# Kernel optimization log

Measured on AMD Instinct MI355X. Metric: run time of the kernel, lower is better.

## Reference

```python
import jax, jax.numpy as jnp
import numpy as np

EPS = 1e-6
LAMB = 0.1
ITERS = 3


def setup_inputs() -> dict:
    key = jax.random.key(0)
    k = jax.random.split(key, 6)
    bi, bt, R, W, D = 128, 128, 36, 50, 1024
    return {
        "img_cls": jax.random.normal(k[0], (bi, D), jnp.float32),
        "imgs": jax.random.normal(k[1], (bi, R, D), jnp.float32),
        "cap_cls": jax.random.normal(k[2], (bt, D), jnp.float32),
        "caps": jax.random.normal(k[3], (bt, W, D), jnp.float32),
        "img_lens": jax.random.randint(k[4], (bi,), 1, R + 1, jnp.int32),
        "cap_lens": jax.random.randint(k[5], (bt,), 1, W + 1, jnp.int32),
    }


def _bregman(cost, mask, r, c):
    # P = exp(-cost/lamb) (masked entries have cost=+inf -> P=0), then
    # iterative row/col rescaling toward marginals r, c.
    P = jnp.where(mask, jnp.exp(-cost / LAMB), 0.0)
    P = P / (jnp.sum(P, axis=(-2, -1), keepdims=True) + EPS)
    for _ in range(ITERS):
        u = P.sum(axis=-1) + EPS          # [bi,bt,R]
        P = P * (r / u)[..., None]
        v = P.sum(axis=-2) + EPS          # [bi,bt,W]
        P = P * (c / v)[:, :, None, :]
    return P


def reference(img_cls, imgs, cap_cls, caps, img_lens, cap_lens):
    imgs = imgs + EPS
    caps = caps + EPS
    # prepend cls token
    imgs = jnp.concatenate([img_cls[:, None, :], imgs], axis=1)   # [bi,R+1,D]
    caps = jnp.concatenate([cap_cls[:, None, :], caps], axis=1)   # [bt,W+1,D]
    imgs = imgs / jnp.linalg.norm(imgs, axis=-1, keepdims=True)
    caps = caps / jnp.linalg.norm(caps, axis=-1, keepdims=True)
    # fine-grained cosine sims: [bi, bt, R+1, W+1]
    fg_sims = jnp.einsum("ird,twd->itrw", imgs, caps)
    il = img_lens + 1
    cl = cap_lens + 1
    R1, W1 = imgs.shape[1], caps.shape[1]
    rmask = jnp.arange(R1)[None, :] < il[:, None]   # [bi,R+1]
    wmask = jnp.arange(W1)[None, :] < cl[:, None]   # [bt,W+1]
    mask = rmask[:, None, :, None] & wmask[None, :, None, :]  # [bi,bt,R+1,W+1]
    # _ave_init: uniform marginals over valid rows/cols
    rvalid = mask.any(axis=-1).astype(fg_sims.dtype)  # [bi,bt,R+1]
    cvalid = mask.any(axis=-2).astype(fg_sims.dtype)  # [bi,bt,W+1]
    r = rvalid / rvalid.sum(axis=-1, keepdims=True)
    c = cvalid / cvalid.sum(axis=-1, keepdims=True)
    cost = 1.0 - fg_sims
    tp = _bregman(cost, mask, r, c)
    sims = jnp.sum(fg_sims * tp * mask.astype(fg_sims.dtype), axis=(-2, -1))
    return sims  # [bi, bt]
```

## Files before the change

kernel.cpp:

```cpp
#include <hip/hip_runtime.h>
#include <hip/hip_fp16.h>

#define EPSF 1e-6f

typedef _Float16 f16x8 __attribute__((ext_vector_type(8)));
typedef float f32x4 __attribute__((ext_vector_type(4)));

#define BK 32
#define SMEM_BYTES 75776
#define BUF_BYTES 10240

#define AS1 __attribute__((address_space(1)))
#define AS3 __attribute__((address_space(3)))

#define VM_WAIT(N) asm volatile("s_waitcnt vmcnt(" #N ")" ::: "memory")
#define LGKM0()    asm volatile("s_waitcnt lgkmcnt(0)" ::: "memory")

__device__ __forceinline__ float wave_sum_fast(float x) {
    asm volatile(
        "s_nop 1\n\t"
        "v_add_f32 %0, %0, %0 quad_perm:[1,0,3,2] row_mask:0xf bank_mask:0xf bound_ctrl:0\n\t"
        "s_nop 1\n\t"
        "v_add_f32 %0, %0, %0 quad_perm:[2,3,0,1] row_mask:0xf bank_mask:0xf bound_ctrl:0\n\t"
        "s_nop 1\n\t"
        "v_add_f32 %0, %0, %0 row_half_mirror row_mask:0xf bank_mask:0xf bound_ctrl:0\n\t"
        "s_nop 1\n\t"
        "v_add_f32 %0, %0, %0 row_mirror row_mask:0xf bank_mask:0xf bound_ctrl:0\n\t"
        "s_nop 1\n\t"
        "v_add_f32 %0, %0, %0 row_bcast:15 row_mask:0xf bank_mask:0xf bound_ctrl:0\n\t"
        "s_nop 1\n\t"
        "v_add_f32 %0, %0, %0 row_bcast:31 row_mask:0xf bank_mask:0xf bound_ctrl:0"
        : "+v"(x));
    return __int_as_float(__builtin_amdgcn_readlane(__float_as_int(x), 63));
}

__global__ __launch_bounds__(256) void norm_kernel(
        const float* __restrict__ img_cls, const float* __restrict__ imgs,
        const float* __restrict__ cap_cls, const float* __restrict__ caps,
        __half* __restrict__ Ah, __half* __restrict__ Bh) {
    __shared__ float red[4];
    const int row = blockIdx.x;
    const int tid = threadIdx.x;

    const float* src = nullptr;
    __half* dsth;
    float eps_add = EPSF;
    if (row < 64 * 80) {
        const int g = row / 80, r = row % 80;
        dsth = Ah + (size_t)row * 1024 + tid * 4;
        int i = -1, rr = 0;
        if (r < 37)      { i = 2 * g;     rr = r; }
        else if (r < 74) { i = 2 * g + 1; rr = r - 37; }
        if (i >= 0) {
            if (rr == 0) { src = img_cls + (size_t)i * 1024; eps_add = 0.0f; }
            else         { src = imgs + ((size_t)i * 36 + (rr - 1)) * 1024; }
        }
    } else {
        const int row2 = row - 64 * 80;
        const int t = row2 >> 6, r = row2 & 63;
        const int n = r >> 4, fr = r & 15;
        const int kt = tid >> 3, q4 = (tid >> 1) & 3, j = (tid & 1) * 4;
        dsth = Bh + ((size_t)(t * 32 + kt) * 4 + n) * 512 + (q4 * 16 + fr) * 8 + j;
        if (r == 0)       { src = cap_cls + (size_t)t * 1024; eps_add = 0.0f; }
        else if (r <= 50) { src = caps + ((size_t)t * 50 + (r - 1)) * 1024; }
    }

    if (src == nullptr) {
        ushort4 z; z.x = z.y = z.z = z.w = 0;
        *reinterpret_cast<ushort4*>(dsth) = z;
        return;
    }

    float4 v = reinterpret_cast<const float4*>(src)[tid];
    v.x += eps_add; v.y += eps_add; v.z += eps_add; v.w += eps_add;
    float ss = v.x * v.x + v.y * v.y + v.z * v.z + v.w * v.w;
    #pragma unroll
    for (int m = 1; m <= 32; m <<= 1) ss += __shfl_xor(ss, m);
    if ((tid & 63) == 0) red[tid >> 6] = ss;
    __syncthreads();
    const float tot = red[0] + red[1] + red[2] + red[3];
    const float rn = 1.0f / sqrtf(tot);

    ushort4 o;
    o.x = __half_as_ushort(__float2half(v.x * rn));
    o.y = __half_as_ushort(__float2half(v.y * rn));
    o.z = __half_as_ushort(__float2half(v.z * rn));
    o.w = __half_as_ushort(__float2half(v.w * rn));
    *reinterpret_cast<ushort4*>(dsth) = o;
}

__device__ __forceinline__ void stage_octA(const __half* __restrict__ Ag,
                                           __half* buf, int kb, int o, size_t lofs) {
    const __half* src = Ag + (size_t)o * 16384 + kb + lofs;
    __builtin_amdgcn_global_load_lds((const AS1 void*)src,
                                     (AS3 void*)(buf + o * 512), 16, 0, 0);
}

__device__ __forceinline__ void stage_A(const __half* __restrict__ Ag,
                                        __half* buf, int kb, int wave, size_t lofs) {
    stage_octA(Ag, buf, kb, wave, lofs);
    if (wave < 2) stage_octA(Ag, buf, kb, wave + 8, lofs);
}

__device__ __forceinline__ void ds_af(const __half* buf, int wm2, int fr, int q4,
                                      f16x8 af[5]) {
    const int soff = ((q4 ^ ((fr >> 1) & 3)) * 8);
    #pragma unroll
    for (int m = 0; m < 5; ++m) {
        const int R = wm2 * 80 + m * 16 + fr;
        af[m] = *reinterpret_cast<const f16x8*>(buf + R * BK + soff);
    }
}

__device__ __forceinline__ void load_bf(const __half* __restrict__ Bgw, int kt,
                                        f16x8 bf[2]) {
    const __half* p = Bgw + (size_t)kt * 2048;
    bf[0] = *reinterpret_cast<const f16x8*>(p);
    bf[1] = *reinterpret_cast<const f16x8*>(p + 512);
}

__device__ __forceinline__ void mfma_cluster(f32x4 acc[5][2], const f16x8 af[5],
                                             const f16x8 bf[2]) {
    __builtin_amdgcn_s_setprio(1);
    #pragma unroll
    for (int m = 0; m < 5; ++m)
        #pragma unroll
        for (int n = 0; n < 2; ++n)
            acc[m][n] = __builtin_amdgcn_mfma_f32_16x16x32_f16(af[m], bf[n], acc[m][n], 0, 0, 0);
    __builtin_amdgcn_s_setprio(0);
}

__global__ __launch_bounds__(512, 4) void fused_kernel(
        const __half* __restrict__ Ah, const __half* __restrict__ Bh,
        const int* __restrict__ img_lens, const int* __restrict__ cap_lens,
        float* __restrict__ out) {
    __shared__ __align__(16) char smem[SMEM_BYTES];
    __half* lds0 = reinterpret_cast<__half*>(smem);
    __half* lds1 = reinterpret_cast<__half*>(smem + BUF_BYTES);
    __half* lds2 = reinterpret_cast<__half*>(smem + 2 * BUF_BYTES);
    __half* lds3 = reinterpret_cast<__half*>(smem + 3 * BUF_BYTES);

    const int idx = blockIdx.x;
    const int xcd = idx & 7;
    const int within = idx >> 3;
    const int bx = within >> 3;
    const int by = xcd * 8 + (within & 7);

    const int tid = threadIdx.x;
    const int wave = tid >> 6;
    const int lane = tid & 63;
    const int wm2 = wave >> 2;
    const int wn2 = wave & 3;
    const int fr = lane & 15;
    const int q4 = lane >> 4;

    const __half* Ag = Ah + (size_t)bx * 160 * 1024;
    const __half* Bgw = Bh + (size_t)(2 * by + (wn2 >> 1)) * 65536
                           + (size_t)((wn2 & 1) * 2) * 512 + lane * 8;

    const int rsub = lane >> 2;
    const int segsrc = (lane & 3) ^ ((lane >> 3) & 3);
    const size_t lofs = (size_t)rsub * 1024 + (size_t)(segsrc * 8);

    f32x4 acc[5][2];
    #pragma unroll
    for (int m = 0; m < 5; ++m)
        #pragma unroll
        for (int n = 0; n < 2; ++n) {
            f32x4 z = {0.0f, 0.0f, 0.0f, 0.0f};
            acc[m][n] = z;
        }

    f16x8 bfA[2], bfB[2];

    stage_A(Ag, lds0, 0, wave, lofs);
    load_bf(Bgw, 0, bfA);
    stage_A(Ag, lds1, BK, wave, lofs);
    load_bf(Bgw, 1, bfB);
    stage_A(Ag, lds2, 2 * BK, wave, lofs);
    if (wave < 2) { VM_WAIT(6); } else { VM_WAIT(4); }
    __builtin_amdgcn_s_barrier();

    #define GEMM_TILE(KT, RDBUF, STBUF, CUR)                          \
    {                                                                 \
        f16x8 af[5];                                                  \
        ds_af((RDBUF), wm2, fr, q4, af);                              \
        mfma_cluster(acc, af, (CUR));                                 \
        load_bf(Bgw, (KT) + 2, (CUR));                                \
        LGKM0();                                                      \
        stage_A(Ag, (STBUF), ((KT) + 3) * BK, wave, lofs);            \
        if (wave < 2) { VM_WAIT(6); } else { VM_WAIT(4); }            \
        __builtin_amdgcn_s_barrier();                                 \
    }

    #pragma unroll 1
    for (int kt = 0; kt < 28; kt += 4) {
        GEMM_TILE(kt,     lds0, lds3, bfA);
        GEMM_TILE(kt + 1, lds1, lds0, bfB);
        GEMM_TILE(kt + 2, lds2, lds1, bfA);
        GEMM_TILE(kt + 3, lds3, lds2, bfB);
    }
    GEMM_TILE(28, lds0, lds3, bfA);
    #undef GEMM_TILE

    {
        f16x8 af[5];
        ds_af(lds1, wm2, fr, q4, af);
        mfma_cluster(acc, af, bfB);
        load_bf(Bgw, 31, bfB);
        LGKM0();
        if (wave < 2) { VM_WAIT(4); } else { VM_WAIT(3); }
        __builtin_amdgcn_s_barrier();
    }
    {
        f16x8 af[5];
        ds_af(lds2, wm2, fr, q4, af);
        mfma_cluster(acc, af, bfA);
        LGKM0();
        VM_WAIT(2);
        __builtin_amdgcn_s_barrier();
    }
    {
        f16x8 af[5];
        ds_af(lds3, wm2, fr, q4, af);
        VM_WAIT(0);
        mfma_cluster(acc, af, bfB);
    }

    __syncthreads();

    float* fgall = reinterpret_cast<float*>(smem);
    const int tt = wn2 >> 1;
    {
        #pragma unroll
        for (int m = 0; m < 5; ++m) {
            #pragma unroll
            for (int q = 0; q < 4; ++q) {
                const int Rl = m * 16 + q4 * 4 + q;
                const int s = (Rl >= 37) ? 1 : 0;
                const int sr = Rl - 37 * s;
                const bool valid = (Rl < 74);
                const int rg = (wm2 * 2 + s) * 2 + tt;
                const int sw = ((sr >> 2) & 3) << 4;
                #pragma unroll
                for (int n = 0; n < 2; ++n) {
                    const int sc = (wn2 & 1) * 32 + n * 16 + fr;
                    if (valid)
                        fgall[rg * 2368 + sr * 64 + (sc ^ sw)] = acc[m][n][q];
                }
            }
        }
    }
    __syncthreads();

    {
        float* fg = fgall + wave * 2368;
        const int i = 4 * bx + (wave >> 1);
        const int t = 2 * by + (wave & 1);
        const int il = img_lens[i] + 1;
        const int cl = cap_lens[t] + 1;
        const bool vcol = lane < cl;

        #define FGR(r_) fg[(r_) * 64 + (lane ^ ((((r_) >> 2) & 3) << 4))]
        #define CEND(c_) ((((c_) * 8 + 8) < 37) ? ((c_) * 8 + 8) : 37)

        float P[37];
        #pragma unroll
        for (int r = 0; r < 37; ++r) P[r] = 0.0f;

        float ts[4] = {0.f, 0.f, 0.f, 0.f};
        #pragma unroll
        for (int c = 0; c < 5; ++c) {
            if (c * 8 < il) {
                #pragma unroll
                for (int r = c * 8; r < CEND(c); ++r) {
                    const float f = FGR(r);
                    const bool act = (r < il) && vcol;
                    const float pe = act ? __expf((f - 1.0f) * 10.0f) : 0.0f;
                    P[r] = pe;
                    ts[r & 3] += pe;
                }
            }
        }
        float tot = (ts[0] + ts[1]) + (ts[2] + ts[3]);
        tot = wave_sum_fast(tot);
        const float s0 = __builtin_amdgcn_rcpf(tot + EPSF);
        #pragma unroll
        for (int c = 0; c < 5; ++c) {
            if (c * 8 < il) {
                #pragma unroll
                for (int r = c * 8; r < CEND(c); ++r) P[r] *= s0;
            }
        }

        const float rmarg = 1.0f / (float)il;
        const float cmarg = 1.0f / (float)cl;
        float csave = 0.0f;
        for (int it = 0; it < 3; ++it) {
            #pragma unroll
            for (int c = 0; c < 5; ++c) {
                if (c * 8 < il) {
                    #pragma unroll
                    for (int r = c * 8; r < CEND(c); ++r) {
                        const float u = wave_sum_fast(P[r]);
                        P[r] *= rmarg * __builtin_amdgcn_rcpf(u + EPSF);
                    }
                }
            }
            float vs[4] = {EPSF, 0.f, 0.f, 0.f};
            #pragma unroll
            for (int c = 0; c < 5; ++c) {
                if (c * 8 < il) {
                    #pragma unroll
                    for (int r = c * 8; r < CEND(c); ++r) vs[r & 3] += P[r];
                }
            }
            const float v = (vs[0] + vs[1]) + (vs[2] + vs[3]);
            const float cs = vcol ? cmarg * __builtin_amdgcn_rcpf(v) : 0.0f;
            if (it < 2) {
                #pragma unroll
                for (int c = 0; c < 5; ++c) {
                    if (c * 8 < il) {
                        #pragma unroll
                        for (int r = c * 8; r < CEND(c); ++r) P[r] *= cs;
                    }
                }
            } else {
                csave = cs;
            }
        }

        float ls[4] = {0.f, 0.f, 0.f, 0.f};
        #pragma unroll
        for (int c = 0; c < 5; ++c) {
            if (c * 8 < il) {
                #pragma unroll
                for (int r = c * 8; r < CEND(c); ++r) {
                    const float f = FGR(r);
                    const float fm = (r < il) ? f : 0.0f;
                    ls[r & 3] = fmaf(fm, P[r], ls[r & 3]);
                }
            }
        }
        float local = csave * ((ls[0] + ls[1]) + (ls[2] + ls[3]));
        local = wave_sum_fast(local);
        if (lane == 0) out[i * 128 + t] = local;
        #undef FGR
        #undef CEND
    }
}

extern "C" void kernel_launch(void* const* d_in, const int* in_sizes, int n_in,
                              void* d_out, int out_size, void* d_ws, size_t ws_size,
                              hipStream_t stream) {
    const float* img_cls  = (const float*)d_in[0];
    const float* imgs     = (const float*)d_in[1];
    const float* cap_cls  = (const float*)d_in[2];
    const float* caps     = (const float*)d_in[3];
    const int*   img_lens = (const int*)d_in[4];
    const int*   cap_lens = (const int*)d_in[5];
    float* out = (float*)d_out;

    __half* Ah = (__half*)d_ws;
    __half* Bh = Ah + (size_t)64 * 80 * 1024;

    norm_kernel<<<64 * 80 + 128 * 64, 256, 0, stream>>>(img_cls, imgs, cap_cls, caps, Ah, Bh);
    fused_kernel<<<2048, 512, 0, stream>>>(Ah, Bh, img_lens, cap_lens, out);
}
```

Baseline: 148.5 us.

## Double GEMM K-tile to 64 with triple-buffered LDS staging

```diff
diff --git a/kernel.cpp b/kernel.cpp
--- a/kernel.cpp
+++ b/kernel.cpp
@@ -6,9 +6,9 @@
 typedef _Float16 f16x8 __attribute__((ext_vector_type(8)));
 typedef float f32x4 __attribute__((ext_vector_type(4)));
 
-#define BK 32
+#define BK 64
 #define SMEM_BYTES 75776
-#define BUF_BYTES 10240
+#define BUF_BYTES 20480
 
 #define AS1 __attribute__((address_space(1)))
 #define AS3 __attribute__((address_space(3)))
@@ -91,7 +91,7 @@
 
 __device__ __forceinline__ void stage_octA(const __half* __restrict__ Ag,
                                            __half* buf, int kb, int o, size_t lofs) {
-    const __half* src = Ag + (size_t)o * 16384 + kb + lofs;
+    const __half* src = Ag + (size_t)o * 8192 + kb + lofs;
     __builtin_amdgcn_global_load_lds((const AS1 void*)src,
                                      (AS3 void*)(buf + o * 512), 16, 0, 0);
 }
@@ -99,12 +99,14 @@
 __device__ __forceinline__ void stage_A(const __half* __restrict__ Ag,
                                         __half* buf, int kb, int wave, size_t lofs) {
     stage_octA(Ag, buf, kb, wave, lofs);
-    if (wave < 2) stage_octA(Ag, buf, kb, wave + 8, lofs);
-}
-
+    stage_octA(Ag, buf, kb, wave + 8, lofs);
+    if (wave < 4) stage_octA(Ag, buf, kb, wave + 16, lofs);
+}
+
+template <int KS>
 __device__ __forceinline__ void ds_af(const __half* buf, int wm2, int fr, int q4,
                                       f16x8 af[5]) {
-    const int soff = ((q4 ^ ((fr >> 1) & 3)) * 8);
+    const int soff = (((KS * 4 + q4) ^ (fr & 7)) * 8);
     #pragma unroll
     for (int m = 0; m < 5; ++m) {
         const int R = wm2 * 80 + m * 16 + fr;
@@ -113,20 +115,24 @@
 }
 
 __device__ __forceinline__ void load_bf(const __half* __restrict__ Bgw, int kt,
-                                        f16x8 bf[2]) {
-    const __half* p = Bgw + (size_t)kt * 2048;
+                                        f16x8 bf[4]) {
+    const __half* p = Bgw + (size_t)kt * 4096;
     bf[0] = *reinterpret_cast<const f16x8*>(p);
     bf[1] = *reinterpret_cast<const f16x8*>(p + 512);
-}
-
+    bf[2] = *reinterpret_cast<const f16x8*>(p + 2048);
+    bf[3] = *reinterpret_cast<const f16x8*>(p + 2560);
+}
+
+template <int KS>
 __device__ __forceinline__ void mfma_cluster(f32x4 acc[5][2], const f16x8 af[5],
-                                             const f16x8 bf[2]) {
+                                             const f16x8 bf[4]) {
     __builtin_amdgcn_s_setprio(1);
     #pragma unroll
     for (int m = 0; m < 5; ++m)
         #pragma unroll
         for (int n = 0; n < 2; ++n)
-            acc[m][n] = __builtin_amdgcn_mfma_f32_16x16x32_f16(af[m], bf[n], acc[m][n], 0, 0, 0);
+            acc[m][n] = __builtin_amdgcn_mfma_f32_16x16x32_f16(af[m], bf[KS * 2 + n],
+                                                               acc[m][n], 0, 0, 0);
     __builtin_amdgcn_s_setprio(0);
 }
 
@@ -135,10 +141,9 @@
         const int* __restrict__ img_lens, const int* __restrict__ cap_lens,
         float* __restrict__ out) {
     __shared__ __align__(16) char smem[SMEM_BYTES];
-    __half* lds0 = reinterpret_cast<__half*>(smem);
-    __half* lds1 = reinterpret_cast<__half*>(smem + BUF_BYTES);
-    __half* lds2 = reinterpret_cast<__half*>(smem + 2 * BUF_BYTES);
-    __half* lds3 = reinterpret_cast<__half*>(smem + 3 * BUF_BYTES);
+    __half* ldsb[3] = { reinterpret_cast<__half*>(smem),
+                        reinterpret_cast<__half*>(smem + BUF_BYTES),
+                        reinterpret_cast<__half*>(smem + 2 * BUF_BYTES) };
 
     const int idx = blockIdx.x;
     const int xcd = idx & 7;
@@ -158,9 +163,8 @@
     const __half* Bgw = Bh + (size_t)(2 * by + (wn2 >> 1)) * 65536
                            + (size_t)((wn2 & 1) * 2) * 512 + lane * 8;
 
-    const int rsub = lane >> 2;
-    const int segsrc = (lane & 3) ^ ((lane >> 3) & 3);
-    const size_t lofs = (size_t)rsub * 1024 + (size_t)(segsrc * 8);
+    const int segsrc = (lane & 7) ^ (lane >> 3);
+    const size_t lofs = (size_t)(lane >> 3) * 1024 + (size_t)(segsrc * 8);
 
     f32x4 acc[5][2];
     #pragma unroll
@@ -171,60 +175,58 @@
             acc[m][n] = z;
         }
 
-    f16x8 bfA[2], bfB[2];
-
-    stage_A(Ag, lds0, 0, wave, lofs);
+    f16x8 bfA[4], bfB[4];
+
     load_bf(Bgw, 0, bfA);
-    stage_A(Ag, lds1, BK, wave, lofs);
+    stage_A(Ag, ldsb[0], 0, wave, lofs);
     load_bf(Bgw, 1, bfB);
-    stage_A(Ag, lds2, 2 * BK, wave, lofs);
-    if (wave < 2) { VM_WAIT(6); } else { VM_WAIT(4); }
+    stage_A(Ag, ldsb[1], BK, wave, lofs);
+    if (wave < 4) { VM_WAIT(7); } else { VM_WAIT(6); }
     __builtin_amdgcn_s_barrier();
 
-    #define GEMM_TILE(KT, RDBUF, STBUF, CUR)                          \
+    #define GEMM_TILE(KT, RD, ST, CUR)                                \
     {                                                                 \
         f16x8 af[5];                                                  \
-        ds_af((RDBUF), wm2, fr, q4, af);                              \
-        mfma_cluster(acc, af, (CUR));                                 \
+        ds_af<0>((RD), wm2, fr, q4, af);                              \
+        mfma_cluster<0>(acc, af, (CUR));                              \
+        ds_af<1>((RD), wm2, fr, q4, af);                              \
+        mfma_cluster<1>(acc, af, (CUR));                              \
         load_bf(Bgw, (KT) + 2, (CUR));                                \
         LGKM0();                                                      \
-        stage_A(Ag, (STBUF), ((KT) + 3) * BK, wave, lofs);            \
-        if (wave < 2) { VM_WAIT(6); } else { VM_WAIT(4); }            \
+        stage_A(Ag, (ST), ((KT) + 2) * BK, wave, lofs);               \
+        if (wave < 4) { VM_WAIT(7); } else { VM_WAIT(6); }            \
         __builtin_amdgcn_s_barrier();                                 \
     }
 
     #pragma unroll 1
-    for (int kt = 0; kt < 28; kt += 4) {
-        GEMM_TILE(kt,     lds0, lds3, bfA);
-        GEMM_TILE(kt + 1, lds1, lds0, bfB);
-        GEMM_TILE(kt + 2, lds2, lds1, bfA);
-        GEMM_TILE(kt + 3, lds3, lds2, bfB);
-    }
-    GEMM_TILE(28, lds0, lds3, bfA);
+    for (int kt = 0; kt < 12; kt += 6) {
+        GEMM_TILE(kt,     ldsb[0], ldsb[2], bfA);
+        GEMM_TILE(kt + 1, ldsb[1], ldsb[0], bfB);
+        GEMM_TILE(kt + 2, ldsb[2], ldsb[1], bfA);
+        GEMM_TILE(kt + 3, ldsb[0], ldsb[2], bfB);
+        GEMM_TILE(kt + 4, ldsb[1], ldsb[0], bfA);
+        GEMM_TILE(kt + 5, ldsb[2], ldsb[1], bfB);
+    }
+    GEMM_TILE(12, ldsb[0], ldsb[2], bfA);
+    GEMM_TILE(13, ldsb[1], ldsb[0], bfB);
     #undef GEMM_TILE
 
     {
         f16x8 af[5];
-        ds_af(lds1, wm2, fr, q4, af);
-        mfma_cluster(acc, af, bfB);
-        load_bf(Bgw, 31, bfB);
+        ds_af<0>(ldsb[2], wm2, fr, q4, af);
+        mfma_cluster<0>(acc, af, bfA);
+        ds_af<1>(ldsb[2], wm2, fr, q4, af);
+        mfma_cluster<1>(acc, af, bfA);
         LGKM0();
-        if (wave < 2) { VM_WAIT(4); } else { VM_WAIT(3); }
+        VM_WAIT(0);
         __builtin_amdgcn_s_barrier();
     }
     {
         f16x8 af[5];
-        ds_af(lds2, wm2, fr, q4, af);
-        mfma_cluster(acc, af, bfA);
-        LGKM0();
-        VM_WAIT(2);
-        __builtin_amdgcn_s_barrier();
-    }
-    {
-        f16x8 af[5];
-        ds_af(lds3, wm2, fr, q4, af);
-        VM_WAIT(0);
-        mfma_cluster(acc, af, bfB);
+        ds_af<0>(ldsb[0], wm2, fr, q4, af);
+        mfma_cluster<0>(acc, af, bfB);
+        ds_af<1>(ldsb[0], wm2, fr, q4, af);
+        mfma_cluster<1>(acc, af, bfB);
     }
 
     __syncthreads();
```

Measured after the change: 150.9 us. No clear change (+1.6%).
